# Kernel tuning notes

Hardware: AMD Instinct MI355X
Metric: run time of the kernel (lower is better)

Reference implementation:

```python
import jax, jax.numpy as jnp
import numpy as np

N, E, D_IN, H = 4096, 1024, 256, 64
THETA = 0.01
LN_EPS = 1e-5


def _layer_norm(x, w, b):
    m = x.mean(-1, keepdims=True)
    v = ((x - m) ** 2).mean(-1, keepdims=True)
    return (x - m) * jax.lax.rsqrt(v + LN_EPS) * w + b


def setup_inputs() -> dict:
    key = jax.random.key(0)
    ks = jax.random.split(key, 8)
    xav = lambda k, shp: jax.random.normal(k, shp, jnp.float32) * np.float32(np.sqrt(2.0 / (shp[0] + shp[1])))
    return {
        "adj": jax.random.uniform(ks[0], (N, E), jnp.float32),
        "G": jax.random.normal(ks[1], (N, N), jnp.float32) * 0.02,
        "feats": jax.random.normal(ks[2], (N, D_IN), jnp.float32),
        "W_v_w": xav(ks[3], (H, D_IN)),
        "lin_w": xav(ks[4], (H, D_IN)),
        "w_o_w": xav(ks[5], (1, H)),
        "w_o_b": jnp.zeros((1,), jnp.float32),
        "ln1_w": jnp.ones((H,), jnp.float32),
        "ln1_b": jnp.zeros((H,), jnp.float32),
        "ln2_w": jnp.ones((H,), jnp.float32),
        "ln2_b": jnp.zeros((H,), jnp.float32),
        "kn": 10,
    }


def reference(adj, G, feats, W_v_w, lin_w, w_o_w, w_o_b, ln1_w, ln1_b, ln2_w, ln2_b, kn):
    # adj: (N, E) incidence; torch code transposes then uses adj.t() again,
    # so e_center = feats.T @ adj / edge_degree  -> (D_IN, E)
    e_center = (feats.T @ adj) / adj.sum(0)[None, :]
    f = feats @ W_v_w.T                                   # (N, H) values
    scores = (f @ f.T) / np.float32(np.sqrt(H))           # (N, N)
    attn = jax.nn.softmax(scores, axis=1)
    s = _layer_norm(e_center.T @ lin_w.T, ln1_w, ln1_b)   # (E, H)
    d = _layer_norm(attn @ f, ln2_w, ln2_b)               # (N, H)
    # hadamard_power: scores[m,n] = sum_k w[k]*(s[m,k]-d[n,k])^2 + b
    # expanded to avoid the (E*N, H) broadcast the torch code materializes
    w = w_o_w[0]                                          # (H,)
    ta = ((s * s) @ w)[:, None] + ((d * d) @ w)[None, :] - 2.0 * ((s * w) @ d.T) + w_o_b[0]
    ta = jnp.exp(-ta / np.float32(2 * 20 ** 2))           # (E, N)
    Hm = ta.T                                             # (N, E) soft incidence
    # Generate_G_from_H with unit edge weights, done via row/col scaling
    DV = Hm.sum(1)
    DE = Hm.sum(0)
    invDE = jnp.where(DE > 0, 1.0 / DE, 0.0)
    invDV = jnp.where(DV > 0, DV ** -0.5, 0.0)
    A = (invDV[:, None] * Hm) * invDE[None, :]            # DV2 @ H @ W @ invDE
    B = Hm * invDV[:, None]                               # (DV2 @ H).T side
    G_new = A @ B.T                                       # (N, N)
    return (1.0 - THETA) * G + THETA * G_new
```

## Files before the change

kernel.cpp:

```cpp
#include <hip/hip_runtime.h>
#include <hip/hip_bf16.h>
#include <math.h>

#define NN 4096
#define NE 1024
#define DIN 256
#define HD 64

typedef __hip_bfloat16 bf16;
__device__ __forceinline__ float b2f(bf16 x){ return __bfloat162float(x); }

typedef __attribute__((ext_vector_type(8))) short s16x8;
typedef __attribute__((ext_vector_type(4))) float f32x4;

__device__ __forceinline__ unsigned short f2b_rne(float x){
  unsigned u; __builtin_memcpy(&u, &x, 4);
  u += 0x7fff + ((u>>16)&1);
  return (unsigned short)(u>>16);
}

#define STAGE128(dstbase, PA, strideA, PB, strideB, k0) do{ \
  _Pragma("unroll") \
  for (int it_ = 0; it_ < 4; ++it_){ \
    int r_  = it_*32 + (t>>3); \
    int ss_ = ((t&7) ^ (r_&7))*8; \
    __builtin_amdgcn_global_load_lds( \
      (const __attribute__((address_space(1))) void*)((PA) + (size_t)r_*(strideA) + (k0) + ss_), \
      (__attribute__((address_space(3))) void*)((dstbase) + it_*4096 + t*16), 16, 0, 0); \
    __builtin_amdgcn_global_load_lds( \
      (const __attribute__((address_space(1))) void*)((PB) + (size_t)r_*(strideB) + (k0) + ss_), \
      (__attribute__((address_space(3))) void*)((dstbase) + 16384 + it_*4096 + t*16), 16, 0, 0); \
  } }while(0)

#define COMPUTE64(base) do{ \
  _Pragma("unroll") \
  for (int kk_ = 0; kk_ < 2; ++kk_){ \
    s16x8 a_[4], b_[4]; \
    _Pragma("unroll") \
    for (int mi_ = 0; mi_ < 4; ++mi_){ \
      int row_ = wr*64 + mi_*16 + (lane & 15); \
      int s_   = kk_*4 + (lane >> 4); \
      a_[mi_] = *(const s16x8*)((base) + row_*128 + ((s_ ^ (row_&7))*16)); \
    } \
    _Pragma("unroll") \
    for (int ni_ = 0; ni_ < 4; ++ni_){ \
      int row_ = wc*64 + ni_*16 + (lane & 15); \
      int s_   = kk_*4 + (lane >> 4); \
      b_[ni_] = *(const s16x8*)((base) + 16384 + row_*128 + ((s_ ^ (row_&7))*16)); \
    } \
    _Pragma("unroll") \
    for (int mi_ = 0; mi_ < 4; ++mi_) \
      _Pragma("unroll") \
      for (int ni_ = 0; ni_ < 4; ++ni_) \
        acc[mi_][ni_] = __builtin_amdgcn_mfma_f32_16x16x32_bf16(a_[mi_], b_[ni_], acc[mi_][ni_], 0, 0, 0); \
  } }while(0)

__global__ void k_t2b(const float* __restrict__ src, unsigned short* __restrict__ dst,
                      float* __restrict__ csum){
  __shared__ float Ls[64][65];
  int R = gridDim.x*64, C = gridDim.y*64;
  int r0 = blockIdx.x*64, c0 = blockIdx.y*64;
  int t = threadIdx.x;
  int lr = t>>2, lc = (t&3)*16;
  #pragma unroll
  for (int s = 0; s < 4; ++s){
    float4 v = *(const float4*)(src + (size_t)(r0+lr)*C + c0 + lc + s*4);
    Ls[lr][lc+s*4+0]=v.x; Ls[lr][lc+s*4+1]=v.y; Ls[lr][lc+s*4+2]=v.z; Ls[lr][lc+s*4+3]=v.w;
  }
  __syncthreads();
  if (csum != nullptr && t < 64){
    float s = 0.f;
    #pragma unroll
    for (int r = 0; r < 64; ++r) s += Ls[r][t];
    atomicAdd(&csum[c0 + t], s);
  }
  int wc = t>>3, wr8 = (t&7)*8;
  #pragma unroll
  for (int p = 0; p < 2; ++p){
    int c = wc + p*32;
    s16x8 o;
    #pragma unroll
    for (int e = 0; e < 8; ++e) o[e] = (short)f2b_rne(Ls[wr8+e][c]);
    *(s16x8*)(dst + (size_t)(c0+c)*R + r0 + wr8) = o;
  }
}

__global__ void __launch_bounds__(256, 2)
k_ect_mfma(const unsigned short* __restrict__ fT, const unsigned short* __restrict__ aT,
           float* __restrict__ ecT){
  __shared__ __align__(16) unsigned char sm[65536];
  const int t = threadIdx.x, lane = t & 63, w = t >> 6;
  const int wr = w >> 1, wc = w & 1;
  const int m0 = blockIdx.x*128, n0 = blockIdx.y*128, kb = blockIdx.z*256;
  const unsigned short* PA = fT + (size_t)m0*NN + kb;
  const unsigned short* PB = aT + (size_t)n0*NN + kb;
  f32x4 acc[4][4] = {};
  STAGE128(sm, PA, NN, PB, NN, 0);
  __syncthreads();
  int cur = 0;
  for (int kt = 0; kt < 4; ++kt){
    if (kt < 3) STAGE128(sm + (cur^1)*32768, PA, NN, PB, NN, (kt+1)*64);
    COMPUTE64(sm + cur*32768);
    __syncthreads();
    cur ^= 1;
  }
  #pragma unroll
  for (int mi = 0; mi < 4; ++mi)
    #pragma unroll
    for (int q = 0; q < 4; ++q){
      int c = m0 + wr*64 + mi*16 + (lane>>4)*4 + q;
      #pragma unroll
      for (int ni = 0; ni < 4; ++ni){
        int e = n0 + wc*64 + ni*16 + (lane & 15);
        atomicAdd(&ecT[(size_t)e*DIN + c], acc[mi][ni][q]);
      }
    }
}

__global__ void k_s(const float* __restrict__ ecT, const float* __restrict__ colsum,
                    const float* __restrict__ lin_w,
                    const float* __restrict__ ln1w, const float* __restrict__ ln1b,
                    const float* __restrict__ wow,
                    unsigned short* __restrict__ swb, float* __restrict__ sq_s){
  int e = blockIdx.x, h = threadIdx.x;
  const float* row = ecT + (size_t)e*DIN;
  const float* lw  = lin_w + (size_t)h*DIN;
  float acc = 0.f;
  for (int c = 0; c < DIN; ++c) acc += row[c]*lw[c];
  acc /= colsum[e];
  float tot = acc;
  for (int m=32;m>=1;m>>=1) tot += __shfl_xor(tot,m);
  float mean = tot*(1.f/64.f);
  float dv = acc - mean;
  float vv = dv*dv;
  for (int m=32;m>=1;m>>=1) vv += __shfl_xor(vv,m);
  float y = dv*(1.f/sqrtf(vv*(1.f/64.f)+1e-5f))*ln1w[h] + ln1b[h];
  float wv = wow[h];
  swb[(size_t)e*HD + h] = f2b_rne(y*wv);
  float q = wv*y*y;
  for (int m=32;m>=1;m>>=1) q += __shfl_xor(q,m);
  if (h==0) sq_s[e] = q;
}

__global__ void k_f(const float* __restrict__ feats, const float* __restrict__ Wv,
                    float* __restrict__ f){
  __shared__ float As[64][65];
  __shared__ float Bs[64][65];
  int i0 = blockIdx.x*64;
  int c0 = blockIdx.y*64;
  int tid=threadIdx.x, tx=tid&15, ty=tid>>4;
  float acc[4][4]={};
  for (int idx=tid; idx<4096; idx+=256){
    int r=idx>>6, c=idx&63;
    As[c][r] = feats[(size_t)(i0+r)*DIN + c0+c];
    Bs[c][r] = Wv   [(size_t)r*DIN      + c0+c];
  }
  __syncthreads();
  for (int k=0;k<64;++k){
    float a[4], b[4];
    #pragma unroll
    for (int i=0;i<4;++i) a[i] = As[k][tx*4+i];
    #pragma unroll
    for (int i=0;i<4;++i) b[i] = Bs[k][ty*4+i];
    #pragma unroll
    for (int mi=0;mi<4;++mi)
      #pragma unroll
      for (int ni=0;ni<4;++ni) acc[mi][ni] += a[mi]*b[ni];
  }
  for (int mi=0;mi<4;++mi)
    for (int ni=0;ni<4;++ni)
      atomicAdd(&f[(size_t)(i0+tx*4+mi)*HD + ty*4+ni], acc[mi][ni]);
}

__global__ void k_f2b(const float* __restrict__ f, unsigned short* __restrict__ fb,
                      unsigned short* __restrict__ fbT){
  __shared__ unsigned short Ls[64][72];
  int n0 = blockIdx.x*64;
  int t = threadIdx.x;
  int r = t>>2, c0 = (t&3)*16;
  unsigned short tmp[16];
  #pragma unroll
  for (int s=0;s<16;++s) tmp[s] = f2b_rne(f[(size_t)(n0+r)*HD + c0 + s]);
  s16x8 v0, v1;
  #pragma unroll
  for (int e=0;e<8;++e){ v0[e] = (short)tmp[e]; v1[e] = (short)tmp[8+e]; }
  *(s16x8*)(fb + (size_t)(n0+r)*HD + c0)     = v0;
  *(s16x8*)(fb + (size_t)(n0+r)*HD + c0 + 8) = v1;
  #pragma unroll
  for (int s=0;s<16;++s) Ls[c0+s][r] = tmp[s];
  __syncthreads();
  int h = t>>2, n1 = (t&3)*16;
  s16x8 w0, w1;
  #pragma unroll
  for (int e=0;e<8;++e){ w0[e] = (short)Ls[h][n1+e]; w1[e] = (short)Ls[h][n1+8+e]; }
  *(s16x8*)(fbT + (size_t)h*NN + n0 + n1)     = w0;
  *(s16x8*)(fbT + (size_t)h*NN + n0 + n1 + 8) = w1;
}

__global__ void __launch_bounds__(256)
k_attn(const unsigned short* __restrict__ fb, const unsigned short* __restrict__ fbT,
       float* __restrict__ dpre, float* __restrict__ rowsum){
  __shared__ __align__(16) unsigned char sm[32768];
  const int t  = threadIdx.x;
  const int l  = t & 63;
  const int w  = t >> 6;
  const int g  = l >> 4;
  const int i0 = blockIdx.x*64;
  const int jb0 = blockIdx.y*256;

  s16x8 aQ[2];
  {
    const unsigned short* src = fb + (size_t)(i0 + w*16 + (l&15))*HD + g*8;
    aQ[0] = *(const s16x8*)(src);
    aQ[1] = *(const s16x8*)(src + 32);
  }

  f32x4 acco[4];
  #pragma unroll
  for (int nh=0;nh<4;++nh)
    #pragma unroll
    for (int q=0;q<4;++q) acco[nh][q] = 0.f;
  float rsum[4] = {0.f,0.f,0.f,0.f};

  float* Pw = (float*)(sm + 16384 + w*4096);

  for (int jt = 0; jt < 4; ++jt){
    int j0 = jb0 + jt*64;
    __syncthreads();
    #pragma unroll
    for (int p = 0; p < 2; ++p){
      int r  = p*32 + (t>>3);
      int cs = ((t&7) ^ (r&7))*8;
      __builtin_amdgcn_global_load_lds(
        (const __attribute__((address_space(1))) void*)(fb + (size_t)(j0+r)*HD + cs),
        (__attribute__((address_space(3))) void*)(sm + p*4096 + t*16), 16, 0, 0);
      __builtin_amdgcn_global_load_lds(
        (const __attribute__((address_space(1))) void*)(fbT + (size_t)r*NN + j0 + cs),
        (__attribute__((address_space(3))) void*)(sm + 8192 + p*4096 + t*16), 16, 0, 0);
    }
    __syncthreads();

    f32x4 accs[4];
    #pragma unroll
    for (int nj=0;nj<4;++nj)
      #pragma unroll
      for (int q=0;q<4;++q) accs[nj][q] = 0.f;
    #pragma unroll
    for (int kk=0; kk<2; ++kk){
      int s = kk*4 + g;
      #pragma unroll
      for (int nj=0;nj<4;++nj){
        int row = nj*16 + (l&15);
        s16x8 b = *(const s16x8*)(sm + row*128 + ((s ^ (row&7))*16));
        accs[nj] = __builtin_amdgcn_mfma_f32_16x16x32_bf16(aQ[kk], b, accs[nj], 0,0,0);
      }
    }

    #pragma unroll
    for (int q=0;q<4;++q){
      int i  = g*4 + q;
      int sw = (i&7)<<2;
      #pragma unroll
      for (int nj=0;nj<4;++nj){
        float p = __expf(accs[nj][q]*0.125f);
        rsum[q] += p;
        Pw[i*64 + ((nj*16 + (l&15)) ^ sw)] = p;
      }
    }

    #pragma unroll
    for (int kk=0; kk<2; ++kk){
      int i  = l & 15;
      int sw = (i&7)<<2;
      int jb = g*8 + kk*32;
      f32x4 va = *(const f32x4*)(Pw + i*64 + ( jb      ^ sw));
      f32x4 vb = *(const f32x4*)(Pw + i*64 + ((jb + 4) ^ sw));
      s16x8 pa;
      #pragma unroll
      for (int e=0;e<4;++e){
        float fa = va[e], fbv = vb[e];
        pa[e]   = (short)f2b_rne(fa);
        pa[4+e] = (short)f2b_rne(fbv);
      }
      int s = kk*4 + g;
      #pragma unroll
      for (int nh=0;nh<4;++nh){
        int row = nh*16 + (l&15);
        s16x8 bT = *(const s16x8*)(sm + 8192 + row*128 + ((s ^ (row&7))*16));
        acco[nh] = __builtin_amdgcn_mfma_f32_16x16x32_bf16(pa, bT, acco[nh], 0,0,0);
      }
    }
  }

  #pragma unroll
  for (int q=0;q<4;++q){
    float v = rsum[q];
    v += __shfl_xor(v,1); v += __shfl_xor(v,2);
    v += __shfl_xor(v,4); v += __shfl_xor(v,8);
    if ((l&15)==0) atomicAdd(&rowsum[i0 + w*16 + g*4 + q], v);
  }
  #pragma unroll
  for (int nh=0;nh<4;++nh)
    #pragma unroll
    for (int q=0;q<4;++q)
      atomicAdd(&dpre[(size_t)(i0 + w*16 + g*4 + q)*HD + nh*16 + (l&15)], acco[nh][q]);
}

__global__ void k_dln(const float* __restrict__ dpre, const float* __restrict__ rowsum,
                      const float* __restrict__ ln2w, const float* __restrict__ ln2b,
                      const float* __restrict__ wow,
                      unsigned short* __restrict__ dmatb, float* __restrict__ sq_d){
  int lane = threadIdx.x & 63;
  int n = blockIdx.x*4 + (threadIdx.x>>6);
  float x = dpre[(size_t)n*HD + lane] / rowsum[n];
  float tot = x;
  for (int m=32;m>=1;m>>=1) tot += __shfl_xor(tot,m);
  float mean = tot*(1.f/64.f);
  float dv = x - mean;
  float vv = dv*dv;
  for (int m=32;m>=1;m>>=1) vv += __shfl_xor(vv,m);
  float y = dv*(1.f/sqrtf(vv*(1.f/64.f)+1e-5f))*ln2w[lane] + ln2b[lane];
  dmatb[(size_t)n*HD + lane] = f2b_rne(y);
  float wv = wow[lane];
  float q = wv*y*y;
  for (int m=32;m>=1;m>>=1) q += __shfl_xor(q,m);
  if (lane==0) sq_d[n] = q;
}

__global__ void __launch_bounds__(256)
k_hm(const unsigned short* __restrict__ dmatb, const unsigned short* __restrict__ swb,
     const float* __restrict__ sq_d, const float* __restrict__ sq_s,
     const float* __restrict__ wob, bf16* __restrict__ Hm){
  __shared__ __align__(16) unsigned char sm[8192];
  const int t = threadIdx.x, l = t & 63, w = t >> 6, g = l >> 4;
  const int n0 = blockIdx.x*64, e0 = blockIdx.y*64;
  #pragma unroll
  for (int p = 0; p < 2; ++p){
    int r  = p*32 + (t>>3);
    int cs = ((t&7) ^ (r&7))*8;
    __builtin_amdgcn_global_load_lds(
      (const __attribute__((address_space(1))) void*)(swb + (size_t)(e0+r)*HD + cs),
      (__attribute__((address_space(3))) void*)(sm + p*4096 + t*16), 16, 0, 0);
  }
  s16x8 aQ[2];
  {
    const unsigned short* src = dmatb + (size_t)(n0 + w*16 + (l&15))*HD + g*8;
    aQ[0] = *(const s16x8*)(src);
    aQ[1] = *(const s16x8*)(src + 32);
  }
  f32x4 accs[4];
  #pragma unroll
  for (int nj=0;nj<4;++nj)
    #pragma unroll
    for (int q=0;q<4;++q) accs[nj][q] = 0.f;
  __syncthreads();
  #pragma unroll
  for (int kk=0; kk<2; ++kk){
    int s = kk*4 + g;
    #pragma unroll
    for (int nj=0;nj<4;++nj){
      int row = nj*16 + (l&15);
      s16x8 b = *(const s16x8*)(sm + row*128 + ((s ^ (row&7))*16));
      accs[nj] = __builtin_amdgcn_mfma_f32_16x16x32_bf16(aQ[kk], b, accs[nj], 0,0,0);
    }
  }
  float bias = wob[0];
  float sqd[4];
  #pragma unroll
  for (int q=0;q<4;++q) sqd[q] = sq_d[n0 + w*16 + g*4 + q];
  #pragma unroll
  for (int nj=0;nj<4;++nj){
    int e = e0 + nj*16 + (l&15);
    float sqs = sq_s[e];
    #pragma unroll
    for (int q=0;q<4;++q){
      float ta = sqs + sqd[q] - 2.f*accs[nj][q] + bias;
      float arg = -ta*(1.f/800.f);
      if (!(arg > -88.f)) arg = -88.f;
      if (arg > 60.f)     arg = 60.f;
      int n = n0 + w*16 + g*4 + q;
      Hm[(size_t)n*NE + e] = __float2bfloat16(__expf(arg));
    }
  }
}

__global__ void k_dv(const bf16* __restrict__ Hm, float* __restrict__ invDV){
  __shared__ float sm[256];
  int n = blockIdx.x, t = threadIdx.x;
  const bf16* row = Hm + (size_t)n*NE;
  float a = b2f(row[t]) + b2f(row[t+256]) + b2f(row[t+512]) + b2f(row[t+768]);
  sm[t]=a; __syncthreads();
  for (int s=128;s>0;s>>=1){ if(t<s) sm[t]+=sm[t+s]; __syncthreads(); }
  if (t==0){ float v = sm[0]; invDV[n] = (v>0.f) ? 1.f/sqrtf(v) : 0.f; }
}

__global__ void k_de(const bf16* __restrict__ Hm, float* __restrict__ DE){
  int e  = blockIdx.x*256 + threadIdx.x;
  int i0 = blockIdx.y*128;
  float acc=0.f;
  for (int i=0;i<128;++i) acc += b2f(Hm[(size_t)(i0+i)*NE + e]);
  atomicAdd(&DE[e], acc);
}
__global__ void k_invde(float* __restrict__ DE){
  int e = blockIdx.x*256 + threadIdx.x;
  float v = DE[e];
  DE[e] = (v>0.f) ? rsqrtf(v) : 0.f;
}

__global__ void k_scale(bf16* __restrict__ Hm, const float* __restrict__ rde){
  int idx = blockIdx.x*256 + threadIdx.x;
  int row = idx >> 7, c8 = idx & 127;
  size_t base = (size_t)row*NE + c8*8;
  s16x8 v = *(const s16x8*)(Hm + base);
  s16x8 o;
  #pragma unroll
  for (int j = 0; j < 8; ++j){
    unsigned int ww = ((unsigned int)(unsigned short)v[j]) << 16;
    float fv; __builtin_memcpy(&fv, &ww, 4);
    fv *= rde[c8*8 + j];
    o[j] = (short)f2b_rne(fv);
  }
  *(s16x8*)(Hm + base) = o;
}

__global__ void __launch_bounds__(256, 2)
k_final(const bf16* __restrict__ A2, const float* __restrict__ invDV,
        const float* __restrict__ G, float* __restrict__ out){
  __shared__ __align__(16) unsigned char sm[128*132*4];
  const int t    = threadIdx.x;
  const int lane = t & 63;
  const int w    = t >> 6;
  const int wr   = w >> 1, wc = w & 1;

  int idx = blockIdx.x;
  int bi = (int)(32.5f - sqrtf(32.5f*32.5f - 2.f*(float)idx));
  while ((bi+1)*32 - ((bi+1)*bi)/2 <= idx) ++bi;
  while (bi*32 - (bi*(bi-1))/2 > idx) --bi;
  int bj = bi + (idx - (bi*32 - (bi*(bi-1))/2));
  const int i0 = bi*128, j0 = bj*128;

  const bf16* PA = A2 + (size_t)i0*NE;
  const bf16* PB = A2 + (size_t)j0*NE;

  f32x4 acc[4][4] = {};
  STAGE128(sm, PA, NE, PB, NE, 0);
  __syncthreads();
  int cur = 0;
  for (int kt = 0; kt < 16; ++kt){
    if (kt < 15) STAGE128(sm + (cur^1)*32768, PA, NE, PB, NE, (kt+1)*64);
    COMPUTE64(sm + cur*32768);
    __syncthreads();
    cur ^= 1;
  }

  float dvi[4][4], dvj[4];
  #pragma unroll
  for (int mi = 0; mi < 4; ++mi)
    #pragma unroll
    for (int q = 0; q < 4; ++q)
      dvi[mi][q] = invDV[i0 + wr*64 + mi*16 + (lane>>4)*4 + q];
  #pragma unroll
  for (int ni = 0; ni < 4; ++ni)
    dvj[ni] = invDV[j0 + wc*64 + ni*16 + (lane & 15)];

  float (*T)[132] = (float(*)[132])sm;
  #pragma unroll
  for (int mi = 0; mi < 4; ++mi)
    #pragma unroll
    for (int ni = 0; ni < 4; ++ni)
      #pragma unroll
      for (int q = 0; q < 4; ++q)
        T[wr*64 + mi*16 + (lane>>4)*4 + q][wc*64 + ni*16 + (lane & 15)] =
          0.01f*(dvi[mi][q]*dvj[ni]*acc[mi][ni][q]);
  __syncthreads();

  #pragma unroll
  for (int it = 0; it < 16; ++it){
    int idx2 = it*256 + t;
    int il = idx2 >> 5;
    int jc = (idx2 & 31)*4;
    size_t o = (size_t)(i0+il)*NN + j0 + jc;
    float4 gv = *(const float4*)(G + o);
    float4 r;
    r.x = 0.99f*gv.x + T[il][jc+0];
    r.y = 0.99f*gv.y + T[il][jc+1];
    r.z = 0.99f*gv.z + T[il][jc+2];
    r.w = 0.99f*gv.w + T[il][jc+3];
    *(float4*)(out + o) = r;
  }

  if (bi == bj) return;
  #pragma unroll
  for (int it = 0; it < 16; ++it){
    int idx2 = it*256 + t;
    int jl = idx2 >> 5;
    int ic = (idx2 & 31)*4;
    size_t o = (size_t)(j0+jl)*NN + i0 + ic;
    float4 gv = *(const float4*)(G + o);
    float4 r;
    r.x = 0.99f*gv.x + T[ic+0][jl];
    r.y = 0.99f*gv.y + T[ic+1][jl];
    r.z = 0.99f*gv.z + T[ic+2][jl];
    r.w = 0.99f*gv.w + T[ic+3][jl];
    *(float4*)(out + o) = r;
  }
}

extern "C" void kernel_launch(void* const* d_in, const int* in_sizes, int n_in,
                              void* d_out, int out_size, void* d_ws, size_t ws_size,
                              hipStream_t stream){
  const float* adj  = (const float*)d_in[0];
  const float* G    = (const float*)d_in[1];
  const float* feats= (const float*)d_in[2];
  const float* Wv   = (const float*)d_in[3];
  const float* lin  = (const float*)d_in[4];
  const float* wow  = (const float*)d_in[5];
  const float* wob  = (const float*)d_in[6];
  const float* ln1w = (const float*)d_in[7];
  const float* ln1b = (const float*)d_in[8];
  const float* ln2w = (const float*)d_in[9];
  const float* ln2b = (const float*)d_in[10];
  float* out = (float*)d_out;

  float* w = (float*)d_ws;
  float* colsum = w; w += NE;
  float* DE     = w; w += NE;
  float* sq_s   = w; w += NE;
  float* rowsum = w; w += NN;
  float* sq_d   = w; w += NN;
  float* invDV  = w; w += NN;
  float* ecT    = w; w += NE*DIN;
  float* f      = w; w += NN*HD;
  float* dpre   = w; w += NN*HD;
  unsigned short* swb    = (unsigned short*)w; w += NE*HD/2;
  unsigned short* dmatb  = (unsigned short*)w; w += NN*HD/2;
  unsigned short* fbm    = (unsigned short*)w; w += NN*HD/2;
  unsigned short* fbT    = (unsigned short*)w; w += NN*HD/2;
  unsigned short* featsT = (unsigned short*)w; w += NN*DIN/2;
  bf16*  Hm     = (bf16*)w;
  unsigned short* adjT = (unsigned short*)Hm;

  hipMemsetAsync(colsum, 0, NE*sizeof(float), stream);
  hipMemsetAsync(DE,     0, NE*sizeof(float), stream);
  hipMemsetAsync(rowsum, 0, NN*sizeof(float), stream);
  hipMemsetAsync(ecT,    0, (size_t)NE*DIN*sizeof(float), stream);
  hipMemsetAsync(f,      0, (size_t)NN*HD*sizeof(float), stream);
  hipMemsetAsync(dpre,   0, (size_t)NN*HD*sizeof(float), stream);

  k_t2b     <<<dim3(64,4),   256, 0, stream>>>(feats, featsT, nullptr);
  k_t2b     <<<dim3(64,16),  256, 0, stream>>>(adj, adjT, colsum);
  k_ect_mfma<<<dim3(2,8,16), 256, 0, stream>>>(featsT, adjT, ecT);
  k_s       <<<NE,            64, 0, stream>>>(ecT, colsum, lin, ln1w, ln1b, wow, swb, sq_s);
  k_f       <<<dim3(64,4),   256, 0, stream>>>(feats, Wv, f);
  k_f2b     <<<64,           256, 0, stream>>>(f, fbm, fbT);
  k_attn    <<<dim3(64,16),  256, 0, stream>>>(fbm, fbT, dpre, rowsum);
  k_dln     <<<NN/4,         256, 0, stream>>>(dpre, rowsum, ln2w, ln2b, wow, dmatb, sq_d);
  k_hm      <<<dim3(64,16),  256, 0, stream>>>(dmatb, swb, sq_d, sq_s, wob, Hm);
  k_dv      <<<NN,           256, 0, stream>>>(Hm, invDV);
  k_de      <<<dim3(4,32),   256, 0, stream>>>(Hm, DE);
  k_invde   <<<4,            256, 0, stream>>>(DE);
  k_scale   <<<2048,         256, 0, stream>>>(Hm, DE);
  k_final   <<<528,          256, 0, stream>>>(Hm, invDV, G, out);
}
```

Before: 341.6 us.

## Fuse degree sums into Hm kernel, merge f GEMM with bf16 conversion, double-buffer attn

Merges the f projection and its bf16/transposed conversion into one kernel that loops over the full input dimension, dropping atomics and the f workspace. Computes row and column degree sums inside k_hm via shared and global atomics, removing the k_dv, k_de and k_invde passes over Hm; the reciprocal square roots are now taken in k_scale and k_final. Double-buffers the LDS staging in k_attn so the next tile's load overlaps compute. Also remaps k_final block order and rewrites the transposed tile into LDS for coalesced reads. The trade-offs are more atomic contention in k_hm and more LDS use in k_attn.

```diff
diff --git a/kernel.cpp b/kernel.cpp
--- a/kernel.cpp
+++ b/kernel.cpp
@@ -142,65 +142,75 @@
   if (h==0) sq_s[e] = q;
 }
 
-__global__ void k_f(const float* __restrict__ feats, const float* __restrict__ Wv,
-                    float* __restrict__ f){
+__global__ void k_f_full(const float* __restrict__ feats, const float* __restrict__ Wv,
+                         unsigned short* __restrict__ fb, unsigned short* __restrict__ fbT){
   __shared__ float As[64][65];
   __shared__ float Bs[64][65];
+  __shared__ unsigned short Fs[64][72];
   int i0 = blockIdx.x*64;
-  int c0 = blockIdx.y*64;
   int tid=threadIdx.x, tx=tid&15, ty=tid>>4;
   float acc[4][4]={};
-  for (int idx=tid; idx<4096; idx+=256){
-    int r=idx>>6, c=idx&63;
-    As[c][r] = feats[(size_t)(i0+r)*DIN + c0+c];
-    Bs[c][r] = Wv   [(size_t)r*DIN      + c0+c];
-  }
-  __syncthreads();
-  for (int k=0;k<64;++k){
-    float a[4], b[4];
-    #pragma unroll
-    for (int i=0;i<4;++i) a[i] = As[k][tx*4+i];
-    #pragma unroll
-    for (int i=0;i<4;++i) b[i] = Bs[k][ty*4+i];
-    #pragma unroll
-    for (int mi=0;mi<4;++mi)
-      #pragma unroll
-      for (int ni=0;ni<4;++ni) acc[mi][ni] += a[mi]*b[ni];
-  }
+  for (int c0=0;c0<DIN;c0+=64){
+    if (c0) __syncthreads();
+    for (int idx=tid; idx<4096; idx+=256){
+      int r=idx>>6, c=idx&63;
+      As[c][r] = feats[(size_t)(i0+r)*DIN + c0+c];
+      Bs[c][r] = Wv   [(size_t)r*DIN      + c0+c];
+    }
+    __syncthreads();
+    for (int k=0;k<64;++k){
+      float a[4], b[4];
+      #pragma unroll
+      for (int i=0;i<4;++i) a[i] = As[k][tx*4+i];
+      #pragma unroll
+      for (int i=0;i<4;++i) b[i] = Bs[k][ty*4+i];
+      #pragma unroll
+      for (int mi=0;mi<4;++mi)
+        #pragma unroll
+        for (int ni=0;ni<4;++ni) acc[mi][ni] += a[mi]*b[ni];
+    }
+  }
+  #pragma unroll
   for (int mi=0;mi<4;++mi)
+    #pragma unroll
     for (int ni=0;ni<4;++ni)
-      atomicAdd(&f[(size_t)(i0+tx*4+mi)*HD + ty*4+ni], acc[mi][ni]);
-}
-
-__global__ void k_f2b(const float* __restrict__ f, unsigned short* __restrict__ fb,
-                      unsigned short* __restrict__ fbT){
-  __shared__ unsigned short Ls[64][72];
-  int n0 = blockIdx.x*64;
-  int t = threadIdx.x;
-  int r = t>>2, c0 = (t&3)*16;
-  unsigned short tmp[16];
-  #pragma unroll
-  for (int s=0;s<16;++s) tmp[s] = f2b_rne(f[(size_t)(n0+r)*HD + c0 + s]);
-  s16x8 v0, v1;
-  #pragma unroll
-  for (int e=0;e<8;++e){ v0[e] = (short)tmp[e]; v1[e] = (short)tmp[8+e]; }
-  *(s16x8*)(fb + (size_t)(n0+r)*HD + c0)     = v0;
-  *(s16x8*)(fb + (size_t)(n0+r)*HD + c0 + 8) = v1;
-  #pragma unroll
-  for (int s=0;s<16;++s) Ls[c0+s][r] = tmp[s];
-  __syncthreads();
-  int h = t>>2, n1 = (t&3)*16;
-  s16x8 w0, w1;
-  #pragma unroll
-  for (int e=0;e<8;++e){ w0[e] = (short)Ls[h][n1+e]; w1[e] = (short)Ls[h][n1+8+e]; }
-  *(s16x8*)(fbT + (size_t)h*NN + n0 + n1)     = w0;
-  *(s16x8*)(fbT + (size_t)h*NN + n0 + n1 + 8) = w1;
-}
+      Fs[tx*4+mi][ty*4+ni] = f2b_rne(acc[mi][ni]);
+  __syncthreads();
+  {
+    int r = tid>>2, c0b = (tid&3)*16;
+    s16x8 v0, v1;
+    #pragma unroll
+    for (int e=0;e<8;++e){ v0[e] = (short)Fs[r][c0b+e]; v1[e] = (short)Fs[r][c0b+8+e]; }
+    *(s16x8*)(fb + (size_t)(i0+r)*HD + c0b)     = v0;
+    *(s16x8*)(fb + (size_t)(i0+r)*HD + c0b + 8) = v1;
+  }
+  {
+    int h = tid>>2, n1 = (tid&3)*16;
+    s16x8 w0, w1;
+    #pragma unroll
+    for (int e=0;e<8;++e){ w0[e] = (short)Fs[n1+e][h]; w1[e] = (short)Fs[n1+8+e][h]; }
+    *(s16x8*)(fbT + (size_t)h*NN + i0 + n1)     = w0;
+    *(s16x8*)(fbT + (size_t)h*NN + i0 + n1 + 8) = w1;
+  }
+}
+
+#define STAGE_ATTN(buf, j0s) do{ \
+  _Pragma("unroll") \
+  for (int p_=0;p_<2;++p_){ \
+    int r_  = p_*32 + (t>>3); \
+    int cs_ = ((t&7) ^ (r_&7))*8; \
+    __builtin_amdgcn_global_load_lds( \
+      (const __attribute__((address_space(1))) void*)(fb + (size_t)((j0s)+r_)*HD + cs_), \
+      (__attribute__((address_space(3))) void*)(sm + (buf)*16384 + p_*4096 + t*16), 16, 0, 0); \
+    __builtin_amdgcn_global_load_lds( \
+      (const __attribute__((address_space(1))) void*)(fbT + (size_t)r_*NN + (j0s) + cs_), \
+      (__attribute__((address_space(3))) void*)(sm + (buf)*16384 + 8192 + p_*4096 + t*16), 16, 0, 0); \
+  } }while(0)
 
 __global__ void __launch_bounds__(256)
 k_attn(const unsigned short* __restrict__ fb, const unsigned short* __restrict__ fbT,
        float* __restrict__ dpre, float* __restrict__ rowsum){
-  __shared__ __align__(16) unsigned char sm[32768];
+  __shared__ __align__(16) unsigned char sm[49152];
   const int t  = threadIdx.x;
   const int l  = t & 63;
   const int w  = t >> 6;
@@ -222,23 +232,14 @@
     for (int q=0;q<4;++q) acco[nh][q] = 0.f;
   float rsum[4] = {0.f,0.f,0.f,0.f};
 
-  float* Pw = (float*)(sm + 16384 + w*4096);
-
+  float* Pw = (float*)(sm + 32768 + w*4096);
+
+  STAGE_ATTN(0, jb0);
+  __syncthreads();
+  int cur = 0;
   for (int jt = 0; jt < 4; ++jt){
-    int j0 = jb0 + jt*64;
-    __syncthreads();
-    #pragma unroll
-    for (int p = 0; p < 2; ++p){
-      int r  = p*32 + (t>>3);
-      int cs = ((t&7) ^ (r&7))*8;
-      __builtin_amdgcn_global_load_lds(
-        (const __attribute__((address_space(1))) void*)(fb + (size_t)(j0+r)*HD + cs),
-        (__attribute__((address_space(3))) void*)(sm + p*4096 + t*16), 16, 0, 0);
-      __builtin_amdgcn_global_load_lds(
-        (const __attribute__((address_space(1))) void*)(fbT + (size_t)r*NN + j0 + cs),
-        (__attribute__((address_space(3))) void*)(sm + 8192 + p*4096 + t*16), 16, 0, 0);
-    }
-    __syncthreads();
+    if (jt < 3) STAGE_ATTN(cur^1, jb0 + (jt+1)*64);
+    const unsigned char* B = sm + cur*16384;
 
     f32x4 accs[4];
     #pragma unroll
@@ -251,7 +252,7 @@
       #pragma unroll
       for (int nj=0;nj<4;++nj){
         int row = nj*16 + (l&15);
-        s16x8 b = *(const s16x8*)(sm + row*128 + ((s ^ (row&7))*16));
+        s16x8 b = *(const s16x8*)(B + row*128 + ((s ^ (row&7))*16));
         accs[nj] = __builtin_amdgcn_mfma_f32_16x16x32_bf16(aQ[kk], b, accs[nj], 0,0,0);
       }
     }
@@ -286,10 +287,12 @@
       #pragma unroll
       for (int nh=0;nh<4;++nh){
         int row = nh*16 + (l&15);
-        s16x8 bT = *(const s16x8*)(sm + 8192 + row*128 + ((s ^ (row&7))*16));
+        s16x8 bT = *(const s16x8*)(B + 8192 + row*128 + ((s ^ (row&7))*16));
         acco[nh] = __builtin_amdgcn_mfma_f32_16x16x32_bf16(pa, bT, acco[nh], 0,0,0);
       }
     }
+    __syncthreads();
+    cur ^= 1;
   }
 
   #pragma unroll
@@ -330,8 +333,10 @@
 __global__ void __launch_bounds__(256)
 k_hm(const unsigned short* __restrict__ dmatb, const unsigned short* __restrict__ swb,
      const float* __restrict__ sq_d, const float* __restrict__ sq_s,
-     const float* __restrict__ wob, bf16* __restrict__ Hm){
+     const float* __restrict__ wob, bf16* __restrict__ Hm,
+     float* __restrict__ DE, float* __restrict__ DVacc){
   __shared__ __align__(16) unsigned char sm[8192];
+  __shared__ float DEp[64];
   const int t = threadIdx.x, l = t & 63, w = t >> 6, g = l >> 4;
   const int n0 = blockIdx.x*64, e0 = blockIdx.y*64;
   #pragma unroll
@@ -348,6 +353,7 @@
     aQ[0] = *(const s16x8*)(src);
     aQ[1] = *(const s16x8*)(src + 32);
   }
+  if (t < 64) DEp[t] = 0.f;
   f32x4 accs[4];
   #pragma unroll
   for (int nj=0;nj<4;++nj)
@@ -368,10 +374,12 @@
   float sqd[4];
   #pragma unroll
   for (int q=0;q<4;++q) sqd[q] = sq_d[n0 + w*16 + g*4 + q];
+  float rowp[4] = {0.f,0.f,0.f,0.f};
   #pragma unroll
   for (int nj=0;nj<4;++nj){
     int e = e0 + nj*16 + (l&15);
     float sqs = sq_s[e];
+    float colp = 0.f;
     #pragma unroll
     for (int q=0;q<4;++q){
       float ta = sqs + sqd[q] - 2.f*accs[nj][q] + bias;
@@ -379,35 +387,26 @@
       if (!(arg > -88.f)) arg = -88.f;
       if (arg > 60.f)     arg = 60.f;
       int n = n0 + w*16 + g*4 + q;
-      Hm[(size_t)n*NE + e] = __float2bfloat16(__expf(arg));
-    }
-  }
-}
-
-__global__ void k_dv(const bf16* __restrict__ Hm, float* __restrict__ invDV){
-  __shared__ float sm[256];
-  int n = blockIdx.x, t = threadIdx.x;
-  const bf16* row = Hm + (size_t)n*NE;
-  float a = b2f(row[t]) + b2f(row[t+256]) + b2f(row[t+512]) + b2f(row[t+768]);
-  sm[t]=a; __syncthreads();
-  for (int s=128;s>0;s>>=1){ if(t<s) sm[t]+=sm[t+s]; __syncthreads(); }
-  if (t==0){ float v = sm[0]; invDV[n] = (v>0.f) ? 1.f/sqrtf(v) : 0.f; }
-}
-
-__global__ void k_de(const bf16* __restrict__ Hm, float* __restrict__ DE){
-  int e  = blockIdx.x*256 + threadIdx.x;
-  int i0 = blockIdx.y*128;
-  float acc=0.f;
-  for (int i=0;i<128;++i) acc += b2f(Hm[(size_t)(i0+i)*NE + e]);
-  atomicAdd(&DE[e], acc);
-}
-__global__ void k_invde(float* __restrict__ DE){
-  int e = blockIdx.x*256 + threadIdx.x;
-  float v = DE[e];
-  DE[e] = (v>0.f) ? rsqrtf(v) : 0.f;
-}
-
-__global__ void k_scale(bf16* __restrict__ Hm, const float* __restrict__ rde){
+      bf16 hv = __float2bfloat16(__expf(arg));
+      Hm[(size_t)n*NE + e] = hv;
+      float vr = b2f(hv);
+      rowp[q] += vr;
+      colp    += vr;
+    }
+    atomicAdd(&DEp[nj*16 + (l&15)], colp);
+  }
+  #pragma unroll
+  for (int q=0;q<4;++q){
+    float v = rowp[q];
+    v += __shfl_xor(v,1); v += __shfl_xor(v,2);
+    v += __shfl_xor(v,4); v += __shfl_xor(v,8);
+    if ((l&15)==0) atomicAdd(&DVacc[n0 + w*16 + g*4 + q], v);
+  }
+  __syncthreads();
+  if (t < 64) atomicAdd(&DE[e0 + t], DEp[t]);
+}
+
+__global__ void k_scale(bf16* __restrict__ Hm, const float* __restrict__ DE){
   int idx = blockIdx.x*256 + threadIdx.x;
   int row = idx >> 7, c8 = idx & 127;
   size_t base = (size_t)row*NE + c8*8;
@@ -415,16 +414,18 @@
   s16x8 o;
   #pragma unroll
   for (int j = 0; j < 8; ++j){
+    float de = DE[c8*8 + j];
+    float r  = (de > 0.f) ? rsqrtf(de) : 0.f;
     unsigned int ww = ((unsigned int)(unsigned short)v[j]) << 16;
     float fv; __builtin_memcpy(&fv, &ww, 4);
-    fv *= rde[c8*8 + j];
+    fv *= r;
     o[j] = (short)f2b_rne(fv);
   }
   *(s16x8*)(Hm + base) = o;
 }
 
 __global__ void __launch_bounds__(256, 2)
-k_final(const bf16* __restrict__ A2, const float* __restrict__ invDV,
+k_final(const bf16* __restrict__ A2, const float* __restrict__ DVacc,
         const float* __restrict__ G, float* __restrict__ out){
   __shared__ __align__(16) unsigned char sm[128*132*4];
   const int t    = threadIdx.x;
@@ -432,7 +433,8 @@
   const int w    = t >> 6;
   const int wr   = w >> 1, wc = w & 1;
 
-  int idx = blockIdx.x;
+  int bid = blockIdx.x;
+  int idx = (bid & 7)*66 + (bid >> 3);
   int bi = (int)(32.5f - sqrtf(32.5f*32.5f - 2.f*(float)idx));
   while ((bi+1)*32 - ((bi+1)*bi)/2 <= idx) ++bi;
   while (bi*32 - (bi*(bi-1))/2 > idx) --bi;
@@ -457,11 +459,15 @@
   #pragma unroll
   for (int mi = 0; mi < 4; ++mi)
     #pragma unroll
-    for (int q = 0; q < 4; ++q)
-      dvi[mi][q] = invDV[i0 + wr*64 + mi*16 + (lane>>4)*4 + q];
-  #pragma unroll
-  for (int ni = 0; ni < 4; ++ni)
-    dvj[ni] = invDV[j0 + wc*64 + ni*16 + (lane & 15)];
+    for (int q = 0; q < 4; ++q){
+      float v = DVacc[i0 + wr*64 + mi*16 + (lane>>4)*4 + q];
+      dvi[mi][q] = (v > 0.f) ? rsqrtf(v) : 0.f;
+    }
+  #pragma unroll
+  for (int ni = 0; ni < 4; ++ni){
+    float v = DVacc[j0 + wc*64 + ni*16 + (lane & 15)];
+    dvj[ni] = (v > 0.f) ? rsqrtf(v) : 0.f;
+  }
 
   float (*T)[132] = (float(*)[132])sm;
   #pragma unroll
@@ -490,6 +496,16 @@
   }
 
   if (bi == bj) return;
+  __syncthreads();
+  #pragma unroll
+  for (int mi = 0; mi < 4; ++mi)
+    #pragma unroll
+    for (int ni = 0; ni < 4; ++ni)
+      #pragma unroll
+      for (int q = 0; q < 4; ++q)
+        T[wc*64 + ni*16 + (lane & 15)][wr*64 + mi*16 + (lane>>4)*4 + q] =
+          0.01f*(dvi[mi][q]*dvj[ni]*acc[mi][ni][q]);
+  __syncthreads();
   #pragma unroll
   for (int it = 0; it < 16; ++it){
     int idx2 = it*256 + t;
@@ -498,10 +514,10 @@
     size_t o = (size_t)(j0+jl)*NN + i0 + ic;
     float4 gv = *(const float4*)(G + o);
     float4 r;
-    r.x = 0.99f*gv.x + T[ic+0][jl];
-    r.y = 0.99f*gv.y + T[ic+1][jl];
-    r.z = 0.99f*gv.z + T[ic+2][jl];
-    r.w = 0.99f*gv.w + T[ic+3][jl];
+    r.x = 0.99f*gv.x + T[jl][ic+0];
+    r.y = 0.99f*gv.y + T[jl][ic+1];
+    r.z = 0.99f*gv.z + T[jl][ic+2];
+    r.w = 0.99f*gv.w + T[jl][ic+3];
     *(float4*)(out + o) = r;
   }
 }
@@ -528,9 +544,8 @@
   float* sq_s   = w; w += NE;
   float* rowsum = w; w += NN;
   float* sq_d   = w; w += NN;
-  float* invDV  = w; w += NN;
+  float* DVacc  = w; w += NN;
   float* ecT    = w; w += NE*DIN;
-  float* f      = w; w += NN*HD;
   float* dpre   = w; w += NN*HD;
   unsigned short* swb    = (unsigned short*)w; w += NE*HD/2;
   unsigned short* dmatb  = (unsigned short*)w; w += NN*HD/2;
@@ -543,22 +558,18 @@
   hipMemsetAsync(colsum, 0, NE*sizeof(float), stream);
   hipMemsetAsync(DE,     0, NE*sizeof(float), stream);
   hipMemsetAsync(rowsum, 0, NN*sizeof(float), stream);
+  hipMemsetAsync(DVacc,  0, NN*sizeof(float), stream);
   hipMemsetAsync(ecT,    0, (size_t)NE*DIN*sizeof(float), stream);
-  hipMemsetAsync(f,      0, (size_t)NN*HD*sizeof(float), stream);
   hipMemsetAsync(dpre,   0, (size_t)NN*HD*sizeof(float), stream);
 
   k_t2b     <<<dim3(64,4),   256, 0, stream>>>(feats, featsT, nullptr);
   k_t2b     <<<dim3(64,16),  256, 0, stream>>>(adj, adjT, colsum);
   k_ect_mfma<<<dim3(2,8,16), 256, 0, stream>>>(featsT, adjT, ecT);
   k_s       <<<NE,            64, 0, stream>>>(ecT, colsum, lin, ln1w, ln1b, wow, swb, sq_s);
-  k_f       <<<dim3(64,4),   256, 0, stream>>>(feats, Wv, f);
-  k_f2b     <<<64,           256, 0, stream>>>(f, fbm, fbT);
+  k_f_full  <<<64,           256, 0, stream>>>(feats, Wv, fbm, fbT);
   k_attn    <<<dim3(64,16),  256, 0, stream>>>(fbm, fbT, dpre, rowsum);
   k_dln     <<<NN/4,         256, 0, stream>>>(dpre, rowsum, ln2w, ln2b, wow, dmatb, sq_d);
-  k_hm      <<<dim3(64,16),  256, 0, stream>>>(dmatb, swb, sq_d, sq_s, wob, Hm);
-  k_dv      <<<NN,           256, 0, stream>>>(Hm, invDV);
-  k_de      <<<dim3(4,32),   256, 0, stream>>>(Hm, DE);
-  k_invde   <<<4,            256, 0, stream>>>(DE);
+  k_hm      <<<dim3(64,16),  256, 0, stream>>>(dmatb, swb, sq_d, sq_s, wob, Hm, DE, DVacc);
   k_scale   <<<2048,         256, 0, stream>>>(Hm, DE);
-  k_final   <<<528,          256, 0, stream>>>(Hm, invDV, G, out);
-}
+  k_final   <<<528,          256, 0, stream>>>(Hm, DVacc, G, out);
+}
```

Result: no change. 339.7 us (-0.6%).
